# Performance work log

Measured on AMD Instinct MI355X. Metric: run time of the kernel, lower is better.

The kernel has to match this reference:

```python
import jax, jax.numpy as jnp
import numpy as np

ATT = 64   # attention_size (becomes number of split chunks / effective heads)
NH = 16    # num_heads (becomes chunk width / effective head dim)


def setup_inputs() -> dict:
    key = jax.random.key(0)
    ks = jax.random.split(key, 9)
    B, T, E = 4, 1024, 1024
    AH = ATT * NH  # 1024
    s = 0.02
    return {
        "x": jax.random.normal(ks[0], (B, T, E), jnp.float32),
        "Wq": jax.random.normal(ks[1], (E, AH), jnp.float32) * s,
        "bq": jax.random.normal(ks[2], (AH,), jnp.float32) * s,
        "Wk": jax.random.normal(ks[3], (E, AH), jnp.float32) * s,
        "bk": jax.random.normal(ks[4], (AH,), jnp.float32) * s,
        "Wv": jax.random.normal(ks[5], (E, AH), jnp.float32) * s,
        "bv": jax.random.normal(ks[6], (AH,), jnp.float32) * s,
        "Wo": jax.random.normal(ks[7], (AH, E), jnp.float32) * s,
        "bo": jax.random.normal(ks[8], (E,), jnp.float32) * s,
    }


def reference(x, Wq, bq, Wk, bk, Wv, bv, Wo, bo):
    B, T, E = x.shape
    A, H = ATT, NH

    q = x @ Wq + bq  # [B,T,A*H]
    k = x @ Wk + bk
    v = x @ Wv + bv

    # torch.split(m, num_heads, dim=2) -> A chunks of width H; cat along dim 0
    def split_cat(m):
        # [B,T,A,H] -> [A,B,T,H] -> [A*B,T,H]
        return m.reshape(B, T, A, H).transpose(2, 0, 1, 3).reshape(A * B, T, H)

    q = split_cat(q)
    k = split_cat(k)
    v = split_cat(v)

    scores = jnp.einsum('bqh,bkh->bqk', q, k) / (A ** 0.5)  # [A*B,T,T]
    attn = jax.nn.softmax(scores, axis=-1)
    z = jnp.einsum('bqk,bkh->bqh', attn, v)  # [A*B,T,H]

    # faithful to torch: contiguous [A*B,T,H] viewed as [B, T, A*H] (no un-permute)
    z = z.reshape(B, T, A * H)
    return z @ Wo + bo
```

## Files before the change

### kernel.cpp

```cpp
#include <hip/hip_runtime.h>
#include <hip/hip_bf16.h>


typedef __bf16 bf16_t;
typedef bf16_t bf16x8 __attribute__((ext_vector_type(8)));
typedef short  s16x4 __attribute__((ext_vector_type(4)));
typedef float  f32x4 __attribute__((ext_vector_type(4)));

#define SCALE_LOG2E 0.18033688011112042f

__device__ __forceinline__ void async16(const bf16_t* g, void* l) {
    __builtin_amdgcn_global_load_lds(
        (const __attribute__((address_space(1))) unsigned int*)g,
        (__attribute__((address_space(3))) unsigned int*)l,
        16, 0, 0);
}

__global__ __launch_bounds__(256) void cast_f32_bf16(
    const float* __restrict__ in, bf16_t* __restrict__ out, int n8)
{
    int i = blockIdx.x * 256 + threadIdx.x;
    if (i >= n8) return;
    const float4* p = (const float4*)in + (size_t)i * 2;
    float4 a = p[0], b = p[1];
    bf16x8 o;
    o[0] = (bf16_t)a.x; o[1] = (bf16_t)a.y; o[2] = (bf16_t)a.z; o[3] = (bf16_t)a.w;
    o[4] = (bf16_t)b.x; o[5] = (bf16_t)b.y; o[6] = (bf16_t)b.z; o[7] = (bf16_t)b.w;
    *((bf16x8*)out + i) = o;
}

__global__ __launch_bounds__(256) void transpose_cast(
    const float* __restrict__ W0, const float* __restrict__ W1,
    const float* __restrict__ W2, const float* __restrict__ W3,
    bf16_t* __restrict__ out)
{
    __shared__ float st[32][33];
    const float* W = (blockIdx.z == 0) ? W0 : (blockIdx.z == 1) ? W1
                   : (blockIdx.z == 2) ? W2 : W3;
    bf16_t* o = out + (size_t)blockIdx.z * 1024 * 1024;
    const int n0 = blockIdx.x * 32, k0 = blockIdx.y * 32;
    const int t = threadIdx.x;
    const int r = t >> 3, c4 = (t & 7) * 4;
    float4 v = *(const float4*)(W + (size_t)(k0 + r) * 1024 + n0 + c4);
    st[r][c4 + 0] = v.x; st[r][c4 + 1] = v.y; st[r][c4 + 2] = v.z; st[r][c4 + 3] = v.w;
    __syncthreads();
    bf16_t tmp[4] __attribute__((aligned(8)));
    #pragma unroll
    for (int i = 0; i < 4; ++i) tmp[i] = (bf16_t)st[c4 + i][r];
    *(uint2*)(o + (size_t)(n0 + r) * 1024 + k0 + c4) = *(const uint2*)tmp;
}

template<bool FUSED, int MT>
__global__ __launch_bounds__(256, 3) void gemm_glds(
    const bf16_t* __restrict__ A, const bf16_t* __restrict__ Bt,
    const float* __restrict__ b0, const float* __restrict__ b1,
    const float* __restrict__ b2,
    bf16_t* __restrict__ Qo, bf16_t* __restrict__ Ko, bf16_t* __restrict__ Vo,
    float* __restrict__ Fo)
{
    const int K = 1024;
    __shared__ __align__(16) bf16_t As[MT * 32];
    __shared__ __align__(16) bf16_t Bs[128 * 32];

    constexpr int NTPW = (MT == 128) ? 4 : 2;
    constexpr int JA   = MT / 64;

    const int tid  = threadIdx.x;
    const int wave = tid >> 6;
    const int lane = tid & 63;
    const int quad = lane >> 4;
    const int l16  = lane & 15;
    const int m0 = blockIdx.y * MT;
    const int n0 = blockIdx.x * 128;
    const int wm = (MT == 128) ? (wave >> 1) * 64 : 0;
    const int wn = (MT == 128) ? (wave & 1) * 64 : wave * 32;

    int goffA[JA], goffB[2];
    #pragma unroll
    for (int j = 0; j < JA; ++j) {
        const int row = j * 64 + (tid >> 2);
        const int cl  = (tid & 3) ^ ((row >> 1) & 3);
        goffA[j] = (m0 + row) * K + cl * 8;
    }
    #pragma unroll
    for (int j = 0; j < 2; ++j) {
        const int row = j * 64 + (tid >> 2);
        const int cl  = (tid & 3) ^ ((row >> 1) & 3);
        goffB[j] = (n0 + row) * K + cl * 8;
    }
    const int ldsoff = wave * 1024;

    f32x4 acc[4][NTPW] = {};
    const int sw = (l16 >> 1) & 3;

    for (int k0 = 0; k0 < K; k0 += 32) {
        #pragma unroll
        for (int j = 0; j < JA; ++j)
            async16(A + goffA[j] + k0, (char*)As + j * 4096 + ldsoff);
        #pragma unroll
        for (int j = 0; j < 2; ++j)
            async16(Bt + goffB[j] + k0, (char*)Bs + j * 4096 + ldsoff);
        __syncthreads();

        bf16x8 af[4], bfr[NTPW];
        #pragma unroll
        for (int mt = 0; mt < 4; ++mt)
            af[mt] = *(const bf16x8*)(&As[(wm + mt * 16 + l16) * 32 + (quad ^ sw) * 8]);
        #pragma unroll
        for (int nt = 0; nt < NTPW; ++nt)
            bfr[nt] = *(const bf16x8*)(&Bs[(wn + nt * 16 + l16) * 32 + (quad ^ sw) * 8]);
        #pragma unroll
        for (int mt = 0; mt < 4; ++mt)
            #pragma unroll
            for (int nt = 0; nt < NTPW; ++nt)
                acc[mt][nt] = __builtin_amdgcn_mfma_f32_16x16x32_bf16(
                    af[mt], bfr[nt], acc[mt][nt], 0, 0, 0);
        __syncthreads();
    }

    if (FUSED) {
        const int sel = n0 >> 10;
        const float* bias = (sel == 0) ? b0 : (sel == 1) ? b1 : b2;
        bf16_t* Cout      = (sel == 0) ? Qo : (sel == 1) ? Ko : Vo;
        const float scl   = (sel == 1) ? SCALE_LOG2E : 1.0f;
        const int nb = n0 & 1023;
        #pragma unroll
        for (int nt = 0; nt < NTPW; ++nt) {
            const int n = nb + wn + nt * 16 + l16;
            const float bb = bias[n];
            #pragma unroll
            for (int mt = 0; mt < 4; ++mt)
                #pragma unroll
                for (int i = 0; i < 4; ++i) {
                    const int m = m0 + wm + mt * 16 + quad * 4 + i;
                    Cout[(size_t)m * 1024 + n] = (bf16_t)((acc[mt][nt][i] + bb) * scl);
                }
        }
    } else {
        #pragma unroll
        for (int nt = 0; nt < NTPW; ++nt) {
            const int n = n0 + wn + nt * 16 + l16;
            const float bb = b0[n];
            #pragma unroll
            for (int mt = 0; mt < 4; ++mt)
                #pragma unroll
                for (int i = 0; i < 4; ++i) {
                    const int m = m0 + wm + mt * 16 + quad * 4 + i;
                    Fo[(size_t)m * 1024 + n] = acc[mt][nt][i] + bb;
                }
        }
    }
}

__global__ __launch_bounds__(256, 4) void attn_kernel(
    const bf16_t* __restrict__ Q, const bf16_t* __restrict__ K,
    const bf16_t* __restrict__ V, bf16_t* __restrict__ Z)
{
    __shared__ __align__(16) bf16_t Vt[16][1032];

    const int tid  = threadIdx.x;
    const int wave = tid >> 6;
    const int lane = tid & 63;
    const int quad = lane >> 4;
    const int l16  = lane & 15;
    const int hd = blockIdx.x >> 2;
    const int qc = blockIdx.x & 3;
    const int a = hd >> 2, b = hd & 3;
    const int col0 = a * 16;
    const int qbase = qc * 256 + wave * 64;

    const int r  = tid >> 2;
    const int dq = (tid & 3) * 4;
    const bf16_t* Vp = V + (size_t)(b * 1024 + r) * 1024 + col0 + dq;
    #pragma unroll 4
    for (int t = 0; t < 16; ++t) {
        uint2 vv = *(const uint2*)(Vp + (size_t)(t * 64) * 1024);
        bf16_t t4[4] __attribute__((aligned(8)));
        *(uint2*)t4 = vv;
        #pragma unroll
        for (int ii = 0; ii < 4; ++ii)
            Vt[dq + ii][t * 64 + r] = t4[ii];
    }

    bf16x8 qf[4] = {};
    if (quad < 2) {
        #pragma unroll
        for (int qs = 0; qs < 4; ++qs)
            qf[qs] = *(const bf16x8*)(Q +
                (size_t)(b * 1024 + qbase + qs * 16 + l16) * 1024 + col0 + quad * 8);
    }

    const bf16_t* Kp = K + (size_t)(b * 1024 + l16) * 1024 + col0 + quad * 8;
    bf16x8 kfA[4] = {}, kfB[4] = {};
    if (quad < 2) {
        #pragma unroll
        for (int kt = 0; kt < 4; ++kt)
            kfA[kt] = *(const bf16x8*)(Kp + (size_t)(kt * 16) * 1024);
    }

    __syncthreads();

    const s16x4 ones = { 0x3F80, 0x3F80, 0x3F80, 0x3F80 };

    f32x4 zacc[4] = {};
    f32x4 lacc[4] = {};

#define ATTN_TILE(JIDX, KFCUR, KFNXT, DO_PREFETCH)                            \
    {                                                                         \
        const int j_ = (JIDX);                                                \
        if (DO_PREFETCH && quad < 2) {                                        \
            _Pragma("unroll")                                                 \
            for (int kt = 0; kt < 4; ++kt)                                    \
                KFNXT[kt] = *(const bf16x8*)(                                 \
                    Kp + (size_t)((j_ + 1) * 64 + kt * 16) * 1024);           \
        }                                                                     \
        _Pragma("unroll")                                                     \
        for (int kt = 0; kt < 4; ++kt) {                                      \
            const s16x4 vfrag = __builtin_bit_cast(s16x4,                     \
                *(const uint2*)(&Vt[l16][j_ * 64 + kt * 16 + quad * 4]));     \
            _Pragma("unroll")                                                 \
            for (int qs = 0; qs < 4; ++qs) {                                  \
                f32x4 zc = {0.f, 0.f, 0.f, 0.f};                              \
                f32x4 s = __builtin_amdgcn_mfma_f32_16x16x32_bf16(            \
                    KFCUR[kt], qf[qs], zc, 0, 0, 0);                          \
                unsigned int u0 = __builtin_bit_cast(unsigned int,            \
                    __builtin_amdgcn_exp2f(s[0])) + 0x8000u;                  \
                unsigned int u1 = __builtin_bit_cast(unsigned int,            \
                    __builtin_amdgcn_exp2f(s[1])) + 0x8000u;                  \
                unsigned int u2 = __builtin_bit_cast(unsigned int,            \
                    __builtin_amdgcn_exp2f(s[2])) + 0x8000u;                  \
                unsigned int u3 = __builtin_bit_cast(unsigned int,            \
                    __builtin_amdgcn_exp2f(s[3])) + 0x8000u;                  \
                uint2 w;                                                      \
                w.x = __builtin_amdgcn_perm(u1, u0, 0x07060302u);             \
                w.y = __builtin_amdgcn_perm(u3, u2, 0x07060302u);             \
                const s16x4 pfrag = __builtin_bit_cast(s16x4, w);             \
                zacc[qs] = __builtin_amdgcn_mfma_f32_16x16x16bf16_1k(         \
                    vfrag, pfrag, zacc[qs], 0, 0, 0);                         \
                lacc[qs] = __builtin_amdgcn_mfma_f32_16x16x16bf16_1k(         \
                    ones, pfrag, lacc[qs], 0, 0, 0);                          \
            }                                                                 \
        }                                                                     \
    }

    #pragma unroll 1
    for (int j2 = 0; j2 < 8; ++j2) {
        ATTN_TILE(2 * j2,     kfA, kfB, true)
        ATTN_TILE(2 * j2 + 1, kfB, kfA, (j2 < 7))
    }
#undef ATTN_TILE

    #pragma unroll
    for (int qs = 0; qs < 4; ++qs) {
        const float inv = 1.0f / lacc[qs][0];
        const int q = qbase + qs * 16 + l16;
        bf16_t o4[4] __attribute__((aligned(8)));
        #pragma unroll
        for (int i = 0; i < 4; ++i) o4[i] = (bf16_t)(zacc[qs][i] * inv);
        *(uint2*)(Z + ((size_t)hd * 1024 + q) * 16 + quad * 4) = *(const uint2*)o4;
    }
}

extern "C" void kernel_launch(void* const* d_in, const int* in_sizes, int n_in,
                              void* d_out, int out_size, void* d_ws, size_t ws_size,
                              hipStream_t stream) {
    const float* x  = (const float*)d_in[0];
    const float* Wq = (const float*)d_in[1];
    const float* bq = (const float*)d_in[2];
    const float* Wk = (const float*)d_in[3];
    const float* bk = (const float*)d_in[4];
    const float* Wv = (const float*)d_in[5];
    const float* bv = (const float*)d_in[6];
    const float* Wo = (const float*)d_in[7];
    const float* bo = (const float*)d_in[8];
    float* out = (float*)d_out;

    char* ws = (char*)d_ws;
    bf16_t* x_bf = (bf16_t*)(ws);
    bf16_t* Wt   = (bf16_t*)(ws + (8u << 20));
    bf16_t* Qb   = (bf16_t*)(ws + (16u << 20));
    bf16_t* Kb   = (bf16_t*)(ws + (24u << 20));
    bf16_t* Vb   = (bf16_t*)(ws + (32u << 20));
    bf16_t* Zb   = (bf16_t*)(ws + (40u << 20));
    bf16_t* WtO  = Wt + (size_t)3 * 1024 * 1024;

    cast_f32_bf16<<<dim3(2048), dim3(256), 0, stream>>>(x, x_bf, 524288);
    transpose_cast<<<dim3(32, 32, 4), dim3(256), 0, stream>>>(Wq, Wk, Wv, Wo, Wt);

    gemm_glds<true, 128><<<dim3(24, 32), dim3(256), 0, stream>>>(
        x_bf, Wt, bq, bk, bv, Qb, Kb, Vb, nullptr);

    attn_kernel<<<dim3(1024), dim3(256), 0, stream>>>(Qb, Kb, Vb, Zb);

    gemm_glds<false, 64><<<dim3(8, 64), dim3(256), 0, stream>>>(
        Zb, WtO, bo, nullptr, nullptr, nullptr, nullptr, nullptr, out);
}
```

Before: 192.2 us.

## Split attention key range across two wave groups and combine via LDS

Doubles the attention block to 512 threads, with each group of four waves handling half of the 1024 keys for the same queries. The second group writes its partial numerator and denominator accumulators into LDS, which reuses the V-transpose buffer, and the first group sums them before normalizing and writing Z. This halves the serial key loop per wave to raise wave-level parallelism and latency hiding. It adds a reduction through LDS and extra barriers, and raises per-block resource demand, which may limit how many blocks fit on a CU.

After: 191.3 us. About the same (-0.4%).

```diff
diff --git a/kernel.cpp b/kernel.cpp
--- a/kernel.cpp
+++ b/kernel.cpp
@@ -152,11 +152,13 @@
     }
 }
 
-__global__ __launch_bounds__(256, 4) void attn_kernel(
+__global__ __launch_bounds__(512, 4) void attn_kernel(
     const bf16_t* __restrict__ Q, const bf16_t* __restrict__ K,
     const bf16_t* __restrict__ V, bf16_t* __restrict__ Z)
 {
-    __shared__ __align__(16) bf16_t Vt[16][1032];
+    __shared__ __align__(16) char smem[16 * 1032 * 2];
+    bf16_t (*Vt)[1032] = (bf16_t (*)[1032])smem;
+    float* cmb = (float*)smem;
 
     const int tid  = threadIdx.x;
     const int wave = tid >> 6;
@@ -167,19 +169,22 @@
     const int qc = blockIdx.x & 3;
     const int a = hd >> 2, b = hd & 3;
     const int col0 = a * 16;
-    const int qbase = qc * 256 + wave * 64;
+    const int qw   = wave & 3;
+    const int kvh  = wave >> 2;
+    const int qbase = qc * 256 + qw * 64;
+    const int kb512 = kvh * 512;
 
     const int r  = tid >> 2;
     const int dq = (tid & 3) * 4;
     const bf16_t* Vp = V + (size_t)(b * 1024 + r) * 1024 + col0 + dq;
-    #pragma unroll 4
-    for (int t = 0; t < 16; ++t) {
-        uint2 vv = *(const uint2*)(Vp + (size_t)(t * 64) * 1024);
+    #pragma unroll 2
+    for (int t = 0; t < 8; ++t) {
+        uint2 vv = *(const uint2*)(Vp + (size_t)(t * 128) * 1024);
         bf16_t t4[4] __attribute__((aligned(8)));
         *(uint2*)t4 = vv;
         #pragma unroll
         for (int ii = 0; ii < 4; ++ii)
-            Vt[dq + ii][t * 64 + r] = t4[ii];
+            Vt[dq + ii][t * 128 + r] = t4[ii];
     }
 
     bf16x8 qf[4] = {};
@@ -190,7 +195,7 @@
                 (size_t)(b * 1024 + qbase + qs * 16 + l16) * 1024 + col0 + quad * 8);
     }
 
-    const bf16_t* Kp = K + (size_t)(b * 1024 + l16) * 1024 + col0 + quad * 8;
+    const bf16_t* Kp = K + (size_t)(b * 1024 + kb512 + l16) * 1024 + col0 + quad * 8;
     bf16x8 kfA[4] = {}, kfB[4] = {};
     if (quad < 2) {
         #pragma unroll
@@ -217,7 +222,7 @@
         _Pragma("unroll")                                                     \
         for (int kt = 0; kt < 4; ++kt) {                                      \
             const s16x4 vfrag = __builtin_bit_cast(s16x4,                     \
-                *(const uint2*)(&Vt[l16][j_ * 64 + kt * 16 + quad * 4]));     \
+                *(const uint2*)(&Vt[l16][kb512 + j_ * 64 + kt * 16 + quad * 4])); \
             _Pragma("unroll")                                                 \
             for (int qs = 0; qs < 4; ++qs) {                                  \
                 f32x4 zc = {0.f, 0.f, 0.f, 0.f};                              \
@@ -244,20 +249,35 @@
     }
 
     #pragma unroll 1
-    for (int j2 = 0; j2 < 8; ++j2) {
+    for (int j2 = 0; j2 < 4; ++j2) {
         ATTN_TILE(2 * j2,     kfA, kfB, true)
-        ATTN_TILE(2 * j2 + 1, kfB, kfA, (j2 < 7))
+        ATTN_TILE(2 * j2 + 1, kfB, kfA, (j2 < 3))
     }
 #undef ATTN_TILE
 
-    #pragma unroll
-    for (int qs = 0; qs < 4; ++qs) {
-        const float inv = 1.0f / lacc[qs][0];
-        const int q = qbase + qs * 16 + l16;
-        bf16_t o4[4] __attribute__((aligned(8)));
-        #pragma unroll
-        for (int i = 0; i < 4; ++i) o4[i] = (bf16_t)(zacc[qs][i] * inv);
-        *(uint2*)(Z + ((size_t)hd * 1024 + q) * 16 + quad * 4) = *(const uint2*)o4;
+    __syncthreads();
+    if (wave >= 4) {
+        float* p = cmb + ((size_t)((wave - 4) * 64 + lane)) * 21;
+        #pragma unroll
+        for (int qs = 0; qs < 4; ++qs) {
+            #pragma unroll
+            for (int i = 0; i < 4; ++i) p[qs * 4 + i] = zacc[qs][i];
+            p[16 + qs] = lacc[qs][0];
+        }
+    }
+    __syncthreads();
+    if (wave < 4) {
+        const float* p = cmb + ((size_t)(wave * 64 + lane)) * 21;
+        #pragma unroll
+        for (int qs = 0; qs < 4; ++qs) {
+            const float inv = 1.0f / (lacc[qs][0] + p[16 + qs]);
+            const int q = qbase + qs * 16 + l16;
+            bf16_t o4[4] __attribute__((aligned(8)));
+            #pragma unroll
+            for (int i = 0; i < 4; ++i)
+                o4[i] = (bf16_t)((zacc[qs][i] + p[qs * 4 + i]) * inv);
+            *(uint2*)(Z + ((size_t)hd * 1024 + q) * 16 + quad * 4) = *(const uint2*)o4;
+        }
     }
 }
 
@@ -290,7 +310,7 @@
     gemm_glds<true, 128><<<dim3(24, 32), dim3(256), 0, stream>>>(
         x_bf, Wt, bq, bk, bv, Qb, Kb, Vb, nullptr);
 
-    attn_kernel<<<dim3(1024), dim3(256), 0, stream>>>(Qb, Kb, Vb, Zb);
+    attn_kernel<<<dim3(1024), dim3(512), 0, stream>>>(Qb, Kb, Vb, Zb);
 
     gemm_glds<false, 64><<<dim3(8, 64), dim3(256), 0, stream>>>(
         Zb, WtO, bo, nullptr, nullptr, nullptr, nullptr, nullptr, out);
```
